# Kernel optimization log

Hardware: AMD Instinct MI355X
Metric: run time of the kernel (lower is better)

Reference implementation:

```python
import jax, jax.numpy as jnp
import numpy as np

K = 1024
H = 16
B = 2
T = 2048


def setup_inputs() -> dict:
    key = jax.random.key(0)
    ks = jax.random.split(key, 8)
    x = jax.random.normal(ks[0], (B, T, K), dtype=jnp.float32)
    mask = jax.random.randint(ks[1], (B, T), 0, 2, dtype=jnp.int32)
    scale = 1.0 / np.sqrt(K)
    Wk = jax.random.normal(ks[2], (K, K), dtype=jnp.float32) * scale
    Wq = jax.random.normal(ks[3], (K, K), dtype=jnp.float32) * scale
    Wv = jax.random.normal(ks[4], (K, K), dtype=jnp.float32) * scale
    Wu = jax.random.normal(ks[5], (K, K), dtype=jnp.float32) * scale
    bu = jnp.zeros((K,), dtype=jnp.float32)
    return {"x": x, "mask": mask, "Wk": Wk, "Wq": Wq, "Wv": Wv, "Wu": Wu, "bu": bu}


def reference(x, mask, Wk, Wq, Wv, Wu, bu):
    b, t, k = x.shape
    h = H
    s = k // h
    # Linear(k, k, bias=False): y = x @ W.T
    keys = (x @ Wk.T).reshape(b, t, h, s)
    queries = (x @ Wq.T).reshape(b, t, h, s)
    values = (x @ Wv.T).reshape(b, t, h, s)
    # raw scores [b, h, t, t]; NOTE: original applies NO 1/sqrt(s) scaling
    raw = jnp.einsum("bqhd,bkhd->bhqk", queries, keys)
    # mask [b, t] broadcast over heads and query positions (keys masked)
    raw = jnp.where(mask[:, None, None, :] == 0, -jnp.inf, raw)
    weights = jax.nn.softmax(raw, axis=-1)
    ys = jnp.einsum("bhqk,bkhd->bqhd", weights, values).reshape(b, t, k)
    return ys @ Wu.T + bu
```

## Files before the change

### kernel.cpp

```cpp
#include <hip/hip_runtime.h>
#include <hip/hip_bf16.h>
#include <math.h>

#define TS 2048
#define KD 1024
#define NH 16
#define SD 64
#define MB 4096
#define LOG2E 1.4426950408889634f

typedef __attribute__((ext_vector_type(8))) short bf16x8;
typedef __attribute__((ext_vector_type(4))) short bf16x4;
typedef __attribute__((ext_vector_type(4))) float f32x4;
typedef unsigned short ushort_t;

#define MFMA32(a, b, c) __builtin_amdgcn_mfma_f32_16x16x32_bf16(a, b, c, 0, 0, 0)

union frag8 { bf16x8 v8; bf16x4 h[2]; };

__device__ __forceinline__ ushort_t f2bf_rn(float f) {
    union { __hip_bfloat16 h; ushort_t u; } c;
    c.h = __float2bfloat16(f);
    return c.u;
}
__device__ __forceinline__ float bf2f(ushort_t u) {
    union { unsigned u; float f; } v; v.u = ((unsigned)u) << 16;
    return v.f;
}
__device__ __forceinline__ ushort4 pk4_bf(float a, float b, float c, float d) {
    union { __hip_bfloat162 h; ushort2 u; } x, y;
    x.h = __float22bfloat162_rn(make_float2(a, b));
    y.h = __float22bfloat162_rn(make_float2(c, d));
    return make_ushort4(x.u.x, x.u.y, y.u.x, y.u.y);
}
__device__ __forceinline__ void gload_lds16(const void* g, void* l) {
    __builtin_amdgcn_global_load_lds(
        (const __attribute__((address_space(1))) unsigned int*)g,
        (__attribute__((address_space(3))) unsigned int*)l, 16, 0, 0);
}

__global__ __launch_bounds__(256)
void conv_all(const float* __restrict__ x, const float* __restrict__ wq,
              const float* __restrict__ wk, const float* __restrict__ wv,
              const float* __restrict__ wu,
              ushort_t* XH, ushort_t* XL, ushort_t* WqH, ushort_t* WqL,
              ushort_t* WkH, ushort_t* WkL, ushort_t* WvH, ushort_t* WuH)
{
    int z = blockIdx.y;
    const float* src; ushort_t* H; ushort_t* L = nullptr; int nblk;
    switch (z) {
        case 0:  src = x;  H = XH;  L = XL;  nblk = 4096; break;
        case 1:  src = wq; H = WqH; L = WqL; nblk = 1024; break;
        case 2:  src = wk; H = WkH; L = WkL; nblk = 1024; break;
        case 3:  src = wv; H = WvH;          nblk = 1024; break;
        default: src = wu; H = WuH;          nblk = 1024; break;
    }
    if ((int)blockIdx.x >= nblk) return;
    int idx = blockIdx.x * 256 + threadIdx.x;
    float4 v = ((const float4*)src)[idx];
    if (z == 1) { v.x *= LOG2E; v.y *= LOG2E; v.z *= LOG2E; v.w *= LOG2E; }
    ushort_t h0 = f2bf_rn(v.x), h1 = f2bf_rn(v.y);
    ushort_t h2 = f2bf_rn(v.z), h3 = f2bf_rn(v.w);
    ((ushort4*)H)[idx] = make_ushort4(h0, h1, h2, h3);
    if (L) {
        ushort_t l0 = f2bf_rn(v.x - bf2f(h0)), l1 = f2bf_rn(v.y - bf2f(h1));
        ushort_t l2 = f2bf_rn(v.z - bf2f(h2)), l3 = f2bf_rn(v.w - bf2f(h3));
        ((ushort4*)L)[idx] = make_ushort4(l0, l1, l2, l3);
    }
}

__global__ __launch_bounds__(256)
void gemm_bf16(const ushort_t* __restrict__ Ah, const ushort_t* __restrict__ Al,
               const ushort_t* __restrict__ Bqh, const ushort_t* __restrict__ Bql,
               const ushort_t* __restrict__ Bkh, const ushort_t* __restrict__ Bkl,
               const ushort_t* __restrict__ Bvh, const ushort_t* __restrict__ Buh,
               ushort_t* __restrict__ OQh, ushort_t* __restrict__ OQl,
               ushort_t* __restrict__ OKh, ushort_t* __restrict__ OKl,
               ushort_t* __restrict__ OVt, float* __restrict__ OF,
               const float* __restrict__ bias, int epi_base)
{
    const int epi = epi_base + blockIdx.z;
    const ushort_t* Bh; const ushort_t* Bl = nullptr;
    if      (epi == 0) { Bh = Bqh; Bl = Bql; }
    else if (epi == 1) { Bh = Bkh; Bl = Bkl; }
    else if (epi == 2) { Bh = Bvh; }
    else               { Bh = Buh; }
    const bool terms3 = (epi < 2);

    __shared__ ushort_t sAh[128 * 32];
    __shared__ ushort_t sAl[128 * 32];
    __shared__ ushort_t sBh[128 * 32];
    __shared__ ushort_t sBl[128 * 32];

    const int tid = threadIdx.x;
    const int wave = tid >> 6, lane = tid & 63;
    const int col = lane & 15, quad = lane >> 4;
    const int wm = wave >> 1, wn = wave & 1;
    const int m0 = blockIdx.y * 128, n0 = blockIdx.x * 128;

    f32x4 acc[4][4];
#pragma unroll
    for (int i = 0; i < 4; ++i)
#pragma unroll
        for (int j = 0; j < 4; ++j) acc[i][j] = (f32x4){0.f, 0.f, 0.f, 0.f};

    for (int k0 = 0; k0 < KD; k0 += 32) {
#pragma unroll
        for (int half = 0; half < 2; ++half) {
            int s   = half * 256 + wave * 64 + lane;
            int row = s >> 2, k8 = s & 3;
            int lo  = (half * 256 + wave * 64) * 8;
            gload_lds16(Ah + (size_t)(m0 + row) * KD + k0 + k8 * 8, sAh + lo);
            gload_lds16(Bh + (size_t)(n0 + row) * KD + k0 + k8 * 8, sBh + lo);
            if (terms3) {
                gload_lds16(Al + (size_t)(m0 + row) * KD + k0 + k8 * 8, sAl + lo);
                gload_lds16(Bl + (size_t)(n0 + row) * KD + k0 + k8 * 8, sBl + lo);
            }
        }
        __syncthreads();

        bf16x8 fah[4], fal[4], fbh[4], fbl[4];
#pragma unroll
        for (int j = 0; j < 4; ++j) {
            int ra = (wm * 64 + j * 16 + col) * 32 + quad * 8;
            int rb = (wn * 64 + j * 16 + col) * 32 + quad * 8;
            fah[j] = *(const bf16x8*)&sAh[ra];
            fbh[j] = *(const bf16x8*)&sBh[rb];
            if (terms3) {
                fal[j] = *(const bf16x8*)&sAl[ra];
                fbl[j] = *(const bf16x8*)&sBl[rb];
            }
        }
#pragma unroll
        for (int i = 0; i < 4; ++i) {
            if (terms3) {
#pragma unroll
                for (int j = 0; j < 4; ++j) {
                    acc[i][j] = MFMA32(fah[i], fbh[j], acc[i][j]);
                    acc[i][j] = MFMA32(fah[i], fbl[j], acc[i][j]);
                    acc[i][j] = MFMA32(fal[i], fbh[j], acc[i][j]);
                }
            } else {
#pragma unroll
                for (int j = 0; j < 4; ++j)
                    acc[i][j] = MFMA32(fah[i], fbh[j], acc[i][j]);
            }
        }
        __syncthreads();
    }

    if (epi <= 1) {
        ushort_t* OH = (epi == 0) ? OQh : OKh;
        ushort_t* OL = (epi == 0) ? OQl : OKl;
#pragma unroll
        for (int i = 0; i < 4; ++i) {
            int m = m0 + wm * 64 + i * 16 + quad * 4;
#pragma unroll
            for (int j = 0; j < 4; ++j) {
                int n = n0 + wn * 64 + j * 16 + col;
#pragma unroll
                for (int r = 0; r < 4; ++r) {
                    float v = acc[i][j][r];
                    ushort_t hv = f2bf_rn(v);
                    size_t off = (size_t)(m + r) * KD + n;
                    OH[off] = hv;
                    OL[off] = f2bf_rn(v - bf2f(hv));
                }
            }
        }
    } else if (epi == 2) {
#pragma unroll
        for (int i = 0; i < 4; ++i) {
            int m = m0 + wm * 64 + i * 16 + quad * 4;
            int bb = m >> 11, t = m & (TS - 1);
#pragma unroll
            for (int j = 0; j < 4; ++j) {
                int n = n0 + wn * 64 + j * 16 + col;
                int hh = n >> 6, d = n & 63;
                ushort4 pk = pk4_bf(acc[i][j][0], acc[i][j][1], acc[i][j][2], acc[i][j][3]);
                *(ushort4*)(OVt + ((size_t)(bb * NH + hh) * SD + d) * TS + t) = pk;
            }
        }
    } else {
#pragma unroll
        for (int i = 0; i < 4; ++i) {
            int m = m0 + wm * 64 + i * 16 + quad * 4;
#pragma unroll
            for (int j = 0; j < 4; ++j) {
                int n = n0 + wn * 64 + j * 16 + col;
                float bj = bias[n];
#pragma unroll
                for (int r = 0; r < 4; ++r)
                    OF[(size_t)(m + r) * KD + n] = acc[i][j][r] + bj;
            }
        }
    }
}

__global__ __launch_bounds__(256, 2)
void attn_mfma(const ushort_t* __restrict__ QH, const ushort_t* __restrict__ QL,
               const ushort_t* __restrict__ KH, const ushort_t* __restrict__ KL,
               const ushort_t* __restrict__ VT, const int* __restrict__ mask,
               ushort_t* __restrict__ YH)
{
    const int bh = blockIdx.x;
    const int qt = blockIdx.y;
    const int h  = bh & (NH - 1);
    const int b  = bh >> 4;

    const int tid  = threadIdx.x;
    const int wave = tid >> 6;
    const int lane = tid & 63;
    const int col  = lane & 15;
    const int quad = lane >> 4;

    __shared__ ushort_t smem[12288];
    ushort_t* sKH = smem;
    ushort_t* sKL = smem + 4096;
    ushort_t* sVT = smem + 8192;
    __shared__ float lred[4][64];

    bf16x8 bqh[4][2], bql[4][2];
#pragma unroll
    for (int qf = 0; qf < 4; ++qf) {
        size_t qrow = (size_t)(b * TS + qt * 64 + qf * 16 + col) * KD + h * SD;
#pragma unroll
        for (int c = 0; c < 2; ++c) {
            bqh[qf][c] = *(const bf16x8*)(QH + qrow + c * 32 + quad * 8);
            bql[qf][c] = *(const bf16x8*)(QL + qrow + c * 32 + quad * 8);
        }
    }

    const int l8 = lane >> 3, l7 = lane & 7;
    const ushort_t* gp[6];
    ushort_t* ld[6];
#pragma unroll
    for (int r = 0; r < 6; ++r) {
        int cc  = (r & 1) * 4 + wave;
        int row = cc * 8 + l8;
        int gs  = l7 ^ (row & 7);
        if (r < 2)      gp[r] = KH + (size_t)(b * TS + row) * KD + h * SD + gs * 8;
        else if (r < 4) gp[r] = KL + (size_t)(b * TS + row) * KD + h * SD + gs * 8;
        else            gp[r] = VT + ((size_t)bh * SD + row) * TS + gs * 8;
        ld[r] = ((r < 2) ? sKH : (r < 4) ? sKL : sVT) + cc * 512;
    }
    const int* mp = mask + b * TS + wave * 16 + quad * 4;

    float lp[4] = {0.f, 0.f, 0.f, 0.f};
    f32x4 O[4][4];
#pragma unroll
    for (int dt = 0; dt < 4; ++dt)
#pragma unroll
        for (int qf = 0; qf < 4; ++qf) O[dt][qf] = (f32x4){0.f, 0.f, 0.f, 0.f};

    frag8 av[4], bp4[4];
#pragma unroll
    for (int i = 0; i < 4; ++i) {
        av[i].v8  = (bf16x8){0, 0, 0, 0, 0, 0, 0, 0};
        bp4[i].v8 = (bf16x8){0, 0, 0, 0, 0, 0, 0, 0};
    }

    for (int kt = 0; kt < TS / 64; ++kt) {
#pragma unroll
        for (int r = 0; r < 6; ++r) gload_lds16(gp[r], ld[r]);
        int4 mv = *(const int4*)mp;
        mp += 64;
#pragma unroll
        for (int r = 0; r < 6; ++r) gp[r] += (r < 4) ? 64 * KD : 64;
        __syncthreads();

        f32x4 sinit;
        sinit[0] = mv.x ? 0.f : -INFINITY;
        sinit[1] = mv.y ? 0.f : -INFINITY;
        sinit[2] = mv.z ? 0.f : -INFINITY;
        sinit[3] = mv.w ? 0.f : -INFINITY;

        bf16x8 akh[2], akl[2];
#pragma unroll
        for (int c = 0; c < 2; ++c) {
            int sl = (c * 4 + quad) ^ (col & 7);
            akh[c] = *(const bf16x8*)&sKH[((wave * 16 + col) * 8 + sl) * 8];
            akl[c] = *(const bf16x8*)&sKL[((wave * 16 + col) * 8 + sl) * 8];
        }
#pragma unroll
        for (int dt = 0; dt < 4; ++dt) {
            int sl = (wave * 2 + (quad >> 1)) ^ (col & 7);
            av[dt].h[0] = *(const bf16x4*)&sVT[((dt * 16 + col) * 8 + sl) * 8 + (quad & 1) * 4];
        }

#pragma unroll
        for (int qf = 0; qf < 4; ++qf) {
            f32x4 s1 = sinit;
            f32x4 s2 = (f32x4){0.f, 0.f, 0.f, 0.f};
            s1 = MFMA32(akh[0], bqh[qf][0], s1);
            s2 = MFMA32(akl[0], bqh[qf][0], s2);
            s2 = MFMA32(akh[0], bql[qf][0], s2);
            s1 = MFMA32(akh[1], bqh[qf][1], s1);
            s2 = MFMA32(akl[1], bqh[qf][1], s2);
            s2 = MFMA32(akh[1], bql[qf][1], s2);
            float p0 = exp2f(s1[0] + s2[0]);
            float p1 = exp2f(s1[1] + s2[1]);
            float p2 = exp2f(s1[2] + s2[2]);
            float p3 = exp2f(s1[3] + s2[3]);
            lp[qf] += (p0 + p1) + (p2 + p3);
            union { ushort4 u4; bf16x4 v4; } pk;
            pk.u4 = pk4_bf(p0, p1, p2, p3);
            bp4[qf].h[0] = pk.v4;
        }

#pragma unroll
        for (int dt = 0; dt < 4; ++dt)
#pragma unroll
            for (int qf = 0; qf < 4; ++qf)
                O[dt][qf] = MFMA32(av[dt].v8, bp4[qf].v8, O[dt][qf]);

        __syncthreads();
    }

#pragma unroll
    for (int qf = 0; qf < 4; ++qf) {
        float v = lp[qf];
        v += __shfl_xor(v, 16);
        v += __shfl_xor(v, 32);
        if (lane < 16) lred[wave][qf * 16 + lane] = v;
    }

    float* Of = (float*)smem;
#pragma unroll
    for (int w = 1; w < 4; ++w) {
        __syncthreads();
        if (wave == w) {
#pragma unroll
            for (int dt = 0; dt < 4; ++dt)
#pragma unroll
                for (int qf = 0; qf < 4; ++qf)
                    *(f32x4*)&Of[((dt * 4 + qf) * 64 + lane) * 4] = O[dt][qf];
        }
        __syncthreads();
        if (wave == 0) {
#pragma unroll
            for (int dt = 0; dt < 4; ++dt)
#pragma unroll
                for (int qf = 0; qf < 4; ++qf)
                    O[dt][qf] += *(const f32x4*)&Of[((dt * 4 + qf) * 64 + lane) * 4];
        }
    }
    if (wave == 0) {
        float linv[4];
#pragma unroll
        for (int qf = 0; qf < 4; ++qf) {
            int q = qf * 16 + col;
            linv[qf] = 1.f / (lred[0][q] + lred[1][q] + lred[2][q] + lred[3][q]);
        }
#pragma unroll
        for (int dt = 0; dt < 4; ++dt)
#pragma unroll
            for (int qf = 0; qf < 4; ++qf) {
                ushort4 pk = pk4_bf(O[dt][qf][0] * linv[qf], O[dt][qf][1] * linv[qf],
                                    O[dt][qf][2] * linv[qf], O[dt][qf][3] * linv[qf]);
                *(ushort4*)(YH + (size_t)(b * TS + qt * 64 + qf * 16 + col) * KD +
                            h * SD + dt * 16 + quad * 4) = pk;
            }
    }
}

extern "C" void kernel_launch(void* const* d_in, const int* in_sizes, int n_in,
                              void* d_out, int out_size, void* d_ws, size_t ws_size,
                              hipStream_t stream) {
    const float* x    = (const float*)d_in[0];
    const int*   mask = (const int*)d_in[1];
    const float* Wk   = (const float*)d_in[2];
    const float* Wq   = (const float*)d_in[3];
    const float* Wv   = (const float*)d_in[4];
    const float* Wu   = (const float*)d_in[5];
    const float* bu   = (const float*)d_in[6];
    float* out = (float*)d_out;

    char* w = (char*)d_ws;
    const size_t M1 = (size_t)1 << 20;
    ushort_t* XH  = (ushort_t*)(w);
    ushort_t* XL  = (ushort_t*)(w + 8  * M1);
    ushort_t* WqH = (ushort_t*)(w + 16 * M1);
    ushort_t* WqL = (ushort_t*)(w + 18 * M1);
    ushort_t* WkH = (ushort_t*)(w + 20 * M1);
    ushort_t* WkL = (ushort_t*)(w + 22 * M1);
    ushort_t* WvH = (ushort_t*)(w + 24 * M1);
    ushort_t* QHb = (ushort_t*)(w + 26 * M1);
    ushort_t* QLb = (ushort_t*)(w + 34 * M1);
    ushort_t* KHb = (ushort_t*)(w + 42 * M1);
    ushort_t* KLb = (ushort_t*)(w + 50 * M1);
    ushort_t* WuH = (ushort_t*)(w + 58 * M1);
    ushort_t* VTb = (ushort_t*)d_out;
    ushort_t* YHb = (ushort_t*)(w);

    dim3 blk(256);
    conv_all<<<dim3(4096, 5), blk, 0, stream>>>(x, Wq, Wk, Wv, Wu,
                                                XH, XL, WqH, WqL, WkH, WkL, WvH, WuH);
    gemm_bf16<<<dim3(8, 32, 3), blk, 0, stream>>>(XH, XL, WqH, WqL, WkH, WkL, WvH, WuH,
                                                  QHb, QLb, KHb, KLb, VTb, nullptr,
                                                  nullptr, 0);
    attn_mfma<<<dim3(NH * 2, 32), blk, 0, stream>>>(QHb, QLb, KHb, KLb, VTb, mask, YHb);
    gemm_bf16<<<dim3(8, 32, 1), blk, 0, stream>>>(YHb, nullptr, WqH, WqL, WkH, WkL, WvH, WuH,
                                                  nullptr, nullptr, nullptr, nullptr, nullptr,
                                                  out, bu, 3);
}
```

Baseline: 307.1 us.

## Double-buffer K/V tiles in LDS to overlap loads with MFMA compute

Doubles the shared-memory staging area and prefetches the next key/value tile (plus mask values) into the alternate buffer while the current tile is being computed. This removes the per-iteration wait on global-to-LDS loads before compute. In exchange it doubles LDS use to about 48 KB per block, which may limit occupancy, and the loop drops one of its two barriers per iteration.

```diff
diff --git a/kernel.cpp b/kernel.cpp
--- a/kernel.cpp
+++ b/kernel.cpp
@@ -214,11 +214,12 @@
     const int col  = lane & 15;
     const int quad = lane >> 4;
 
-    __shared__ ushort_t smem[12288];
+    __shared__ ushort_t smem[24576];
     ushort_t* sKH = smem;
     ushort_t* sKL = smem + 4096;
     ushort_t* sVT = smem + 8192;
     __shared__ float lred[4][64];
+    const int BUF = 12288;
 
     bf16x8 bqh[4][2], bql[4][2];
 #pragma unroll
@@ -260,32 +261,45 @@
         bp4[i].v8 = (bf16x8){0, 0, 0, 0, 0, 0, 0, 0};
     }
 
+#pragma unroll
+    for (int r = 0; r < 6; ++r) gload_lds16(gp[r], ld[r]);
+#pragma unroll
+    for (int r = 0; r < 6; ++r) gp[r] += (r < 4) ? 64 * KD : 64;
+    int4 mv_cur = *(const int4*)mp;
+    mp += 64;
+    __syncthreads();
+
+    int cur = 0;
     for (int kt = 0; kt < TS / 64; ++kt) {
-#pragma unroll
-        for (int r = 0; r < 6; ++r) gload_lds16(gp[r], ld[r]);
-        int4 mv = *(const int4*)mp;
-        mp += 64;
-#pragma unroll
-        for (int r = 0; r < 6; ++r) gp[r] += (r < 4) ? 64 * KD : 64;
-        __syncthreads();
+        int4 mv_next;
+        if (kt + 1 < TS / 64) {
+#pragma unroll
+            for (int r = 0; r < 6; ++r)
+                gload_lds16(gp[r], ld[r] + (BUF - cur * BUF));
+#pragma unroll
+            for (int r = 0; r < 6; ++r) gp[r] += (r < 4) ? 64 * KD : 64;
+            mv_next = *(const int4*)mp;
+            mp += 64;
+        }
+        const int co = cur * BUF;
 
         f32x4 sinit;
-        sinit[0] = mv.x ? 0.f : -INFINITY;
-        sinit[1] = mv.y ? 0.f : -INFINITY;
-        sinit[2] = mv.z ? 0.f : -INFINITY;
-        sinit[3] = mv.w ? 0.f : -INFINITY;
+        sinit[0] = mv_cur.x ? 0.f : -INFINITY;
+        sinit[1] = mv_cur.y ? 0.f : -INFINITY;
+        sinit[2] = mv_cur.z ? 0.f : -INFINITY;
+        sinit[3] = mv_cur.w ? 0.f : -INFINITY;
 
         bf16x8 akh[2], akl[2];
 #pragma unroll
         for (int c = 0; c < 2; ++c) {
             int sl = (c * 4 + quad) ^ (col & 7);
-            akh[c] = *(const bf16x8*)&sKH[((wave * 16 + col) * 8 + sl) * 8];
-            akl[c] = *(const bf16x8*)&sKL[((wave * 16 + col) * 8 + sl) * 8];
+            akh[c] = *(const bf16x8*)&sKH[co + ((wave * 16 + col) * 8 + sl) * 8];
+            akl[c] = *(const bf16x8*)&sKL[co + ((wave * 16 + col) * 8 + sl) * 8];
         }
 #pragma unroll
         for (int dt = 0; dt < 4; ++dt) {
             int sl = (wave * 2 + (quad >> 1)) ^ (col & 7);
-            av[dt].h[0] = *(const bf16x4*)&sVT[((dt * 16 + col) * 8 + sl) * 8 + (quad & 1) * 4];
+            av[dt].h[0] = *(const bf16x4*)&sVT[co + ((dt * 16 + col) * 8 + sl) * 8 + (quad & 1) * 4];
         }
 
 #pragma unroll
@@ -315,6 +329,8 @@
                 O[dt][qf] = MFMA32(av[dt].v8, bp4[qf].v8, O[dt][qf]);
 
         __syncthreads();
+        cur ^= 1;
+        mv_cur = mv_next;
     }
 
 #pragma unroll
```

Measured after the change: 309.9 us. No clear change (+0.9%).

## Move low-part Q fragments to LDS and raise attention occupancy to three blocks

Applied to the files above, without the earlier changes.

The low-order bf16 part of Q is now staged once into a swizzled LDS tile and reloaded from shared memory inside each key-tile iteration, instead of being held in registers for the whole kernel. This frees VGPRs so launch bounds can request three blocks per CU instead of two. Global-to-LDS pointer arrays are also replaced with a few scalar offsets to cut register use further. The trade-off is extra LDS reads per iteration and a larger LDS footprint per block, which could itself limit occupancy.

```diff
diff --git a/kernel.cpp b/kernel.cpp
--- a/kernel.cpp
+++ b/kernel.cpp
@@ -197,7 +197,7 @@
     }
 }
 
-__global__ __launch_bounds__(256, 2)
+__global__ __launch_bounds__(256, 3)
 void attn_mfma(const ushort_t* __restrict__ QH, const ushort_t* __restrict__ QL,
                const ushort_t* __restrict__ KH, const ushort_t* __restrict__ KL,
                const ushort_t* __restrict__ VT, const int* __restrict__ mask,
@@ -214,36 +214,38 @@
     const int col  = lane & 15;
     const int quad = lane >> 4;
 
-    __shared__ ushort_t smem[12288];
+    __shared__ ushort_t smem[16384];
     ushort_t* sKH = smem;
     ushort_t* sKL = smem + 4096;
     ushort_t* sVT = smem + 8192;
+    ushort_t* sQL = smem + 12288;
     __shared__ float lred[4][64];
 
-    bf16x8 bqh[4][2], bql[4][2];
+    bf16x8 bqh[4][2];
 #pragma unroll
     for (int qf = 0; qf < 4; ++qf) {
         size_t qrow = (size_t)(b * TS + qt * 64 + qf * 16 + col) * KD + h * SD;
 #pragma unroll
-        for (int c = 0; c < 2; ++c) {
+        for (int c = 0; c < 2; ++c)
             bqh[qf][c] = *(const bf16x8*)(QH + qrow + c * 32 + quad * 8);
-            bql[qf][c] = *(const bf16x8*)(QL + qrow + c * 32 + quad * 8);
+    }
+    {
+        int s = tid;
+#pragma unroll
+        for (int p = 0; p < 2; ++p, s += 256) {
+            int row = s >> 3, dblk = s & 7;
+            bf16x8 v = *(const bf16x8*)(QL + (size_t)(b * TS + qt * 64 + row) * KD +
+                                        h * SD + dblk * 8);
+            *(bf16x8*)((char*)sQL + ((row * 128 + dblk * 16) ^ ((row & 7) << 4))) = v;
         }
     }
 
     const int l8 = lane >> 3, l7 = lane & 7;
-    const ushort_t* gp[6];
-    ushort_t* ld[6];
-#pragma unroll
-    for (int r = 0; r < 6; ++r) {
-        int cc  = (r & 1) * 4 + wave;
-        int row = cc * 8 + l8;
-        int gs  = l7 ^ (row & 7);
-        if (r < 2)      gp[r] = KH + (size_t)(b * TS + row) * KD + h * SD + gs * 8;
-        else if (r < 4) gp[r] = KL + (size_t)(b * TS + row) * KD + h * SD + gs * 8;
-        else            gp[r] = VT + ((size_t)bh * SD + row) * TS + gs * 8;
-        ld[r] = ((r < 2) ? sKH : (r < 4) ? sKL : sVT) + cc * 512;
-    }
+    const int gs = (l7 ^ l8) * 8;
+    const int aK = (wave * 8 + l8) * KD + gs;
+    const int aV = (bh * SD + wave * 8 + l8) * TS + gs;
+    size_t kOff = (size_t)b * TS * KD + h * SD;
+    int    vOff = 0;
     const int* mp = mask + b * TS + wave * 16 + quad * 4;
 
     float lp[4] = {0.f, 0.f, 0.f, 0.f};
@@ -261,12 +263,16 @@
     }
 
     for (int kt = 0; kt < TS / 64; ++kt) {
-#pragma unroll
-        for (int r = 0; r < 6; ++r) gload_lds16(gp[r], ld[r]);
+        gload_lds16(KH + kOff + aK,           sKH + wave * 512);
+        gload_lds16(KH + kOff + aK + 32 * KD, sKH + (wave + 4) * 512);
+        gload_lds16(KL + kOff + aK,           sKL + wave * 512);
+        gload_lds16(KL + kOff + aK + 32 * KD, sKL + (wave + 4) * 512);
+        gload_lds16(VT + aV + vOff,           sVT + wave * 512);
+        gload_lds16(VT + aV + vOff + 32 * TS, sVT + (wave + 4) * 512);
         int4 mv = *(const int4*)mp;
         mp += 64;
-#pragma unroll
-        for (int r = 0; r < 6; ++r) gp[r] += (r < 4) ? 64 * KD : 64;
+        kOff += 64 * KD;
+        vOff += 64;
         __syncthreads();
 
         f32x4 sinit;
@@ -290,14 +296,19 @@
 
 #pragma unroll
         for (int qf = 0; qf < 4; ++qf) {
+            int qrow  = qf * 16 + col;
+            int qbase = qrow * 128;
+            int qsw   = (qrow & 7) << 4;
+            bf16x8 bql0 = *(const bf16x8*)((const char*)sQL + qbase + ((quad * 16) ^ qsw));
+            bf16x8 bql1 = *(const bf16x8*)((const char*)sQL + qbase + ((64 + quad * 16) ^ qsw));
             f32x4 s1 = sinit;
             f32x4 s2 = (f32x4){0.f, 0.f, 0.f, 0.f};
             s1 = MFMA32(akh[0], bqh[qf][0], s1);
             s2 = MFMA32(akl[0], bqh[qf][0], s2);
-            s2 = MFMA32(akh[0], bql[qf][0], s2);
+            s2 = MFMA32(akh[0], bql0, s2);
             s1 = MFMA32(akh[1], bqh[qf][1], s1);
             s2 = MFMA32(akl[1], bqh[qf][1], s2);
-            s2 = MFMA32(akh[1], bql[qf][1], s2);
+            s2 = MFMA32(akh[1], bql1, s2);
             float p0 = exp2f(s1[0] + s2[0]);
             float p1 = exp2f(s1[1] + s2[1]);
             float p2 = exp2f(s1[2] + s2[2]);
```

Result: slower. 520.1 us (+69.3%).
